# Kernel optimization log

Hardware: AMD Instinct MI355X
Metric: run time of the kernel (lower is better)

The kernel has to match this reference:

```python
import jax, jax.numpy as jnp
import numpy as np

D_MODEL = 1024
N_HEADS = 16


def setup_inputs() -> dict:
    key = jax.random.key(0)
    ks = jax.random.split(key, 11)
    B, S, D = 2, 2048, D_MODEL
    scale = 1.0 / np.sqrt(D)
    inp = {
        "q": jax.random.normal(ks[0], (B, S, D), jnp.float32),
        "k": jax.random.normal(ks[1], (B, S, D), jnp.float32),
        "v": jax.random.normal(ks[2], (B, S, D), jnp.float32),
        "W_q": jax.random.normal(ks[3], (D, D), jnp.float32) * scale,
        "b_q": jnp.zeros((D,), jnp.float32),
        "W_k": jax.random.normal(ks[4], (D, D), jnp.float32) * scale,
        "b_k": jnp.zeros((D,), jnp.float32),
        "W_v": jax.random.normal(ks[5], (D, D), jnp.float32) * scale,
        "b_v": jnp.zeros((D,), jnp.float32),
        "W_o": jax.random.normal(ks[6], (D, D), jnp.float32) * scale,
        "b_o": jnp.zeros((D,), jnp.float32),
    }
    return inp


def reference(q, k, v, W_q, b_q, W_k, b_k, W_v, b_v, W_o, b_o):
    B, S, D = q.shape
    H = N_HEADS
    d_k = D // H
    # linear projections, then split heads: [B, H, S, d_k]
    def proj(x, W, b):
        y = jnp.einsum("bsd,de->bse", x, W.T) + b
        return y.reshape(B, S, H, d_k).transpose(0, 2, 1, 3)
    Q = proj(q, W_q, b_q)
    K = proj(k, W_k, b_k)
    V = proj(v, W_v, b_v)
    # scaled dot-product attention with explicit [B,H,S,S] scores
    scores = jnp.einsum("bhqd,bhkd->bhqk", Q, K) / jnp.sqrt(jnp.float32(d_k))
    attn = jax.nn.softmax(scores, axis=-1)
    out = jnp.einsum("bhqk,bhkd->bhqd", attn, V)
    out = out.transpose(0, 2, 1, 3).reshape(B, S, D)
    return jnp.einsum("bsd,de->bse", out, W_o.T) + b_o
```

## Files before the change

kernel.cpp:

```cpp
#include <hip/hip_runtime.h>
#include <hip/hip_bf16.h>
#include <math.h>

typedef __bf16 bf16_t;
typedef bf16_t bf16x8 __attribute__((ext_vector_type(8)));
typedef float f32x4 __attribute__((ext_vector_type(4)));

#define D_MODEL 1024
#define NH 16
#define DK 64
#define SEQ 2048
#define MROWS 4096
#define LDSW 64
#define LDC 136

__device__ __forceinline__ bf16x8 ldfrag(const bf16_t* p) {
    union { uint4 u; bf16x8 v; } c;
    c.u = *reinterpret_cast<const uint4*>(p);
    return c.v;
}

__device__ __forceinline__ f32x4 zero4() { f32x4 z = {0.f, 0.f, 0.f, 0.f}; return z; }

__device__ __forceinline__ void gll16(const bf16_t* g, bf16_t* l) {
    __builtin_amdgcn_global_load_lds(
        (const __attribute__((address_space(1))) unsigned int*)g,
        (__attribute__((address_space(3))) unsigned int*)l,
        16, 0, 0);
}

__global__ void pack7(const float* __restrict__ q, const float* __restrict__ k,
                      const float* __restrict__ v, const float* __restrict__ wq,
                      const float* __restrict__ wk, const float* __restrict__ wv,
                      const float* __restrict__ wo,
                      bf16_t* __restrict__ dq, bf16_t* __restrict__ dk,
                      bf16_t* __restrict__ dv, bf16_t* __restrict__ dwq,
                      bf16_t* __restrict__ dwk, bf16_t* __restrict__ dwv,
                      bf16_t* __restrict__ dwo) {
    const int y = blockIdx.y;
    if (y >= 3 && blockIdx.x >= 1024) return;
    const float* s;
    bf16_t* d;
    switch (y) {
        case 0: s = q;  d = dq;  break;
        case 1: s = k;  d = dk;  break;
        case 2: s = v;  d = dv;  break;
        case 3: s = wq; d = dwq; break;
        case 4: s = wk; d = dwk; break;
        case 5: s = wv; d = dwv; break;
        default: s = wo; d = dwo; break;
    }
    int i = (blockIdx.x * blockDim.x + threadIdx.x) * 4;
    float4 f = *reinterpret_cast<const float4*>(s + i);
    union { bf16_t h[4]; uint2 u; } o;
    o.h[0] = (bf16_t)f.x; o.h[1] = (bf16_t)f.y; o.h[2] = (bf16_t)f.z; o.h[3] = (bf16_t)f.w;
    *reinterpret_cast<uint2*>(d + i) = o.u;
}

__device__ __forceinline__ void gemm_core(
    const bf16_t* __restrict__ A, const bf16_t* __restrict__ Bm,
    int K, int m0, int n0,
    bf16_t* As, bf16_t* Bs,
    f32x4 acc[4][4]) {

    const int tid = threadIdx.x;
    const int lane = tid & 63;
    const int wid = tid >> 6;
    const int wm = (wid >> 1) * 64, wn = (wid & 1) * 64;
    const int l15 = lane & 15, quad = lane >> 4;

    const int lrow   = lane >> 3;
    const int gcol   = ((lane & 7) ^ lrow) * 8;

    #pragma unroll
    for (int i = 0; i < 4; i++)
        #pragma unroll
        for (int j = 0; j < 4; j++) acc[i][j] = zero4();

    for (int k0 = 0; k0 < K; k0 += 64) {
        __syncthreads();
        #pragma unroll
        for (int t = 0; t < 4; t++) {
            const int rbase = wid * 32 + t * 8;
            gll16(A  + (size_t)(m0 + rbase + lrow) * K + k0 + gcol, As + rbase * LDSW);
            gll16(Bm + (size_t)(n0 + rbase + lrow) * K + k0 + gcol, Bs + rbase * LDSW);
        }
        __syncthreads();
        #pragma unroll
        for (int c = 0; c < 2; c++) {
            bf16x8 af[4], bfr[4];
            #pragma unroll
            for (int i = 0; i < 4; i++) {
                const int row = wm + i * 16 + l15;
                const int pc = ((c * 4 + quad) ^ (l15 & 7)) * 8;
                af[i] = ldfrag(As + row * LDSW + pc);
            }
            #pragma unroll
            for (int j = 0; j < 4; j++) {
                const int row = wn + j * 16 + l15;
                const int pc = ((c * 4 + quad) ^ (l15 & 7)) * 8;
                bfr[j] = ldfrag(Bs + row * LDSW + pc);
            }
            #pragma unroll
            for (int i = 0; i < 4; i++)
                #pragma unroll
                for (int j = 0; j < 4; j++)
                    acc[i][j] = __builtin_amdgcn_mfma_f32_16x16x32_bf16(af[i], bfr[j], acc[i][j], 0, 0, 0);
        }
    }
}

__global__ __launch_bounds__(256, 3) void proj_gemm(
    const bf16_t* __restrict__ qb, const bf16_t* __restrict__ kb,
    const bf16_t* __restrict__ vb,
    const bf16_t* __restrict__ Wq, const bf16_t* __restrict__ Wk,
    const bf16_t* __restrict__ Wv,
    const float* __restrict__ bq, const float* __restrict__ bk, const float* __restrict__ bv,
    bf16_t* __restrict__ Qh, bf16_t* __restrict__ Kh, bf16_t* __restrict__ Vt) {

    __shared__ __align__(16) bf16_t sm[128 * LDC];
    bf16_t* As = sm;
    bf16_t* Bs = sm + 128 * LDSW;
    bf16_t (*Cs)[LDC] = reinterpret_cast<bf16_t(*)[LDC]>(sm);
    f32x4 acc[4][4];

    const int mode = blockIdx.z;
    const bf16_t* X = (mode == 0) ? qb : (mode == 1) ? kb : vb;
    const bf16_t* W = (mode == 0) ? Wq : (mode == 1) ? Wk : Wv;
    const float* bias = (mode == 0) ? bq : (mode == 1) ? bk : bv;
    const int m0 = blockIdx.y * 128, n0 = blockIdx.x * 128;

    gemm_core(X, W, D_MODEL, m0, n0, As, Bs, acc);

    const int tid = threadIdx.x, lane = tid & 63, wid = tid >> 6;
    const int wm = (wid >> 1) * 64, wn = (wid & 1) * 64;
    const int l15 = lane & 15, quad = lane >> 4;

    __syncthreads();
    if (mode != 2) {
        const float sc = (mode == 0) ? 0.125f * 1.44269504f : 1.0f;
        #pragma unroll
        for (int i = 0; i < 4; i++)
            #pragma unroll
            for (int j = 0; j < 4; j++)
                #pragma unroll
                for (int r = 0; r < 4; r++) {
                    int gn = n0 + wn + j * 16 + l15;
                    Cs[wm + i * 16 + quad * 4 + r][wn + j * 16 + l15] =
                        (bf16_t)((acc[i][j][r] + bias[gn]) * sc);
                }
    } else {
        #pragma unroll
        for (int i = 0; i < 4; i++)
            #pragma unroll
            for (int j = 0; j < 4; j++)
                #pragma unroll
                for (int r = 0; r < 4; r++) {
                    int gn = n0 + wn + j * 16 + l15;
                    Cs[wn + j * 16 + l15][wm + i * 16 + quad * 4 + r] =
                        (bf16_t)(acc[i][j][r] + bias[gn]);
                }
    }
    __syncthreads();

    #pragma unroll
    for (int c = tid; c < 2048; c += 256) {
        int row = c >> 4, col8 = (c & 15) << 3;
        uint4 val = *reinterpret_cast<const uint4*>(&Cs[row][col8]);
        if (mode != 2) {
            int gm = m0 + row, gn = n0 + col8;
            int b = gm >> 11, seq = gm & 2047;
            int h = gn >> 6, dk = gn & 63;
            bf16_t* dst = (mode == 0) ? Qh : Kh;
            *reinterpret_cast<uint4*>(dst + ((size_t)(b * NH + h) * SEQ + seq) * DK + dk) = val;
        } else {
            int gn = n0 + row, gm = m0 + col8;
            int b = gm >> 11, seq = gm & 2047;
            int h = gn >> 6, dk = gn & 63;
            *reinterpret_cast<uint4*>(Vt + ((size_t)(b * NH + h) * DK + dk) * SEQ + seq) = val;
        }
    }
}

__global__ __launch_bounds__(256, 2) void out_gemm(
    const bf16_t* __restrict__ Oc, const bf16_t* __restrict__ Wo,
    const float* __restrict__ bo, float* __restrict__ Cout) {

    __shared__ __align__(16) bf16_t As[64 * LDSW];
    __shared__ __align__(16) bf16_t Bs[128 * LDSW];
    f32x4 acc[2][4];
    const int m0 = blockIdx.y * 64, n0 = blockIdx.x * 128;

    const int tid = threadIdx.x;
    const int lane = tid & 63;
    const int wid = tid >> 6;
    const int wm = (wid >> 1) * 32, wn = (wid & 1) * 64;
    const int l15 = lane & 15, quad = lane >> 4;
    const int lrow = lane >> 3;
    const int gcol = ((lane & 7) ^ lrow) * 8;

    #pragma unroll
    for (int i = 0; i < 2; i++)
        #pragma unroll
        for (int j = 0; j < 4; j++) acc[i][j] = zero4();

    for (int k0 = 0; k0 < D_MODEL; k0 += 64) {
        __syncthreads();
        #pragma unroll
        for (int t = 0; t < 2; t++) {
            const int rbase = wid * 16 + t * 8;
            gll16(Oc + (size_t)(m0 + rbase + lrow) * D_MODEL + k0 + gcol, As + rbase * LDSW);
        }
        #pragma unroll
        for (int t = 0; t < 4; t++) {
            const int rbase = wid * 32 + t * 8;
            gll16(Wo + (size_t)(n0 + rbase + lrow) * D_MODEL + k0 + gcol, Bs + rbase * LDSW);
        }
        __syncthreads();
        #pragma unroll
        for (int c = 0; c < 2; c++) {
            bf16x8 af[2], bfr[4];
            #pragma unroll
            for (int i = 0; i < 2; i++) {
                const int row = wm + i * 16 + l15;
                const int pc = ((c * 4 + quad) ^ (l15 & 7)) * 8;
                af[i] = ldfrag(As + row * LDSW + pc);
            }
            #pragma unroll
            for (int j = 0; j < 4; j++) {
                const int row = wn + j * 16 + l15;
                const int pc = ((c * 4 + quad) ^ (l15 & 7)) * 8;
                bfr[j] = ldfrag(Bs + row * LDSW + pc);
            }
            #pragma unroll
            for (int i = 0; i < 2; i++)
                #pragma unroll
                for (int j = 0; j < 4; j++)
                    acc[i][j] = __builtin_amdgcn_mfma_f32_16x16x32_bf16(af[i], bfr[j], acc[i][j], 0, 0, 0);
        }
    }

    #pragma unroll
    for (int i = 0; i < 2; i++)
        #pragma unroll
        for (int j = 0; j < 4; j++)
            #pragma unroll
            for (int r = 0; r < 4; r++) {
                int gm = m0 + wm + i * 16 + quad * 4 + r;
                int gn = n0 + wn + j * 16 + l15;
                Cout[(size_t)gm * D_MODEL + gn] = acc[i][j][r] + bo[gn];
            }
}

__global__ __launch_bounds__(256) void attn_kernel(
    const bf16_t* __restrict__ Qh, const bf16_t* __restrict__ Kh,
    const bf16_t* __restrict__ Vt, bf16_t* __restrict__ Oc) {

    __shared__ __align__(16) bf16_t Ks[64 * LDSW];
    __shared__ __align__(16) bf16_t Vts[64 * LDSW];
    __shared__ __align__(16) bf16_t Pls[64 * LDSW];

    const int tid = threadIdx.x, lane = tid & 63, wid = tid >> 6;
    const int l15 = lane & 15, quad = lane >> 4;
    const int bh = blockIdx.x;
    const int q0 = blockIdx.y * 64;
    const bf16_t* Qbase = Qh + (size_t)bh * SEQ * DK;
    const bf16_t* Kbase = Kh + (size_t)bh * SEQ * DK;
    const bf16_t* Vbase = Vt + (size_t)bh * DK * SEQ;

    const int lrow = lane >> 3;
    const int gcol = ((lane & 7) ^ lrow) * 8;

    bf16x8 aQ[2];
    #pragma unroll
    for (int c = 0; c < 2; c++)
        aQ[c] = ldfrag(Qbase + (size_t)(q0 + wid * 16 + l15) * DK + c * 32 + quad * 8);

    f32x4 oacc[4];
    #pragma unroll
    for (int j = 0; j < 4; j++) oacc[j] = zero4();
    float l_acc = 0.f;

    const int s7 = l15 & 7;
    bf16_t* prow = Pls + (wid * 16 + l15) * LDSW;

    for (int kt = 0; kt < SEQ / 64; kt++) {
        const int k0 = kt * 64;
        __syncthreads();
        #pragma unroll
        for (int t = 0; t < 2; t++) {
            const int rbase = wid * 16 + t * 8;
            gll16(Kbase + (size_t)(k0 + rbase + lrow) * DK + gcol,  Ks  + rbase * LDSW);
            gll16(Vbase + (size_t)(rbase + lrow) * SEQ + k0 + gcol, Vts + rbase * LDSW);
        }
        __syncthreads();

        f32x4 sacc[4];
        #pragma unroll
        for (int j = 0; j < 4; j++) sacc[j] = zero4();
        #pragma unroll
        for (int c = 0; c < 2; c++) {
            bf16x8 bk4[4];
            #pragma unroll
            for (int j = 0; j < 4; j++) {
                const int pc = ((c * 4 + quad) ^ s7) * 8;
                bk4[j] = ldfrag(Ks + (j * 16 + l15) * LDSW + pc);
            }
            #pragma unroll
            for (int j = 0; j < 4; j++)
                sacc[j] = __builtin_amdgcn_mfma_f32_16x16x32_bf16(
                    bk4[j], aQ[c], sacc[j], 0, 0, 0);
        }

        #pragma unroll
        for (int j = 0; j < 4; j++) {
            float e0 = exp2f(sacc[j][0]);
            float e1 = exp2f(sacc[j][1]);
            float e2 = exp2f(sacc[j][2]);
            float e3 = exp2f(sacc[j][3]);
            l_acc += (e0 + e1) + (e2 + e3);
            union { bf16_t h[4]; unsigned long long u; } pk;
            pk.h[0] = (bf16_t)e0; pk.h[1] = (bf16_t)e1;
            pk.h[2] = (bf16_t)e2; pk.h[3] = (bf16_t)e3;
            const int Lc = j * 2 + (quad >> 1);
            *reinterpret_cast<unsigned long long*>(
                prow + ((Lc ^ s7) << 3) + ((quad & 1) << 2)) = pk.u;
        }

        #pragma unroll
        for (int c = 0; c < 2; c++) {
            bf16x8 ap = ldfrag(prow + (((c * 4 + quad) ^ s7) << 3));
            bf16x8 bv4[4];
            #pragma unroll
            for (int j = 0; j < 4; j++) {
                const int pc = ((c * 4 + quad) ^ s7) * 8;
                bv4[j] = ldfrag(Vts + (j * 16 + l15) * LDSW + pc);
            }
            #pragma unroll
            for (int j = 0; j < 4; j++)
                oacc[j] = __builtin_amdgcn_mfma_f32_16x16x32_bf16(
                    ap, bv4[j], oacc[j], 0, 0, 0);
        }
    }

    float l = l_acc;
    l += __shfl_xor(l, 16, 64);
    l += __shfl_xor(l, 32, 64);

    const int pch = l15 >> 3, pwi = l15 & 7;
    #pragma unroll
    for (int r = 0; r < 4; r++) {
        float lr = __shfl(l, quad * 4 + r, 16);
        float inv = 1.0f / lr;
        bf16_t* orow = Pls + (wid * 16 + quad * 4 + r) * LDSW;
        const int rx = (quad * 4 + r) & 7;
        #pragma unroll
        for (int j = 0; j < 4; j++)
            orow[((pch + 2 * j) ^ rx) * 8 + pwi] = (bf16_t)(oacc[j][r] * inv);
    }
    __syncthreads();

    const int b = bh >> 4, h = bh & 15;
    #pragma unroll
    for (int c = tid; c < 512; c += 256) {
        int row = c >> 3, chunk = c & 7;
        uint4 val = *reinterpret_cast<const uint4*>(
            Pls + row * LDSW + ((chunk ^ (row & 7)) << 3));
        *reinterpret_cast<uint4*>(Oc + ((size_t)(b * SEQ + q0 + row)) * D_MODEL + h * DK + (chunk << 3)) = val;
    }
}

extern "C" void kernel_launch(void* const* d_in, const int* in_sizes, int n_in,
                              void* d_out, int out_size, void* d_ws, size_t ws_size,
                              hipStream_t stream) {
    const float* q  = (const float*)d_in[0];
    const float* k  = (const float*)d_in[1];
    const float* v  = (const float*)d_in[2];
    const float* Wq = (const float*)d_in[3];
    const float* bq = (const float*)d_in[4];
    const float* Wk = (const float*)d_in[5];
    const float* bk = (const float*)d_in[6];
    const float* Wv = (const float*)d_in[7];
    const float* bv = (const float*)d_in[8];
    const float* Wo = (const float*)d_in[9];
    const float* bo = (const float*)d_in[10];

    const size_t nx = (size_t)MROWS * D_MODEL;
    const size_t nw = (size_t)D_MODEL * D_MODEL;

    bf16_t* qb  = (bf16_t*)d_ws;
    bf16_t* kb  = qb  + nx;
    bf16_t* vb  = kb  + nx;
    bf16_t* Wqb = vb  + nx;
    bf16_t* Wkb = Wqb + nw;
    bf16_t* Wvb = Wkb + nw;
    bf16_t* Wob = Wvb + nw;
    bf16_t* Qh  = Wob + nw;
    bf16_t* Kh  = Qh  + nx;
    bf16_t* Vt  = Kh  + nx;
    bf16_t* Oc  = Vt  + nx;

    pack7<<<dim3(4096, 7), 256, 0, stream>>>(q, k, v, Wq, Wk, Wv, Wo,
                                             qb, kb, vb, Wqb, Wkb, Wvb, Wob);

    proj_gemm<<<dim3(8, 32, 3), 256, 0, stream>>>(qb, kb, vb, Wqb, Wkb, Wvb, bq, bk, bv, Qh, Kh, Vt);
    attn_kernel<<<dim3(32, 32), 256, 0, stream>>>(Qh, Kh, Vt, Oc);
    out_gemm<<<dim3(8, 64), 256, 0, stream>>>(Oc, Wob, bo, (float*)d_out);
}
```

Measured before the change: 239.6 us.

## Keep softmax probabilities in registers by permuting K rows to match MFMA layout

Loads K tile rows in a permuted order so the S^T accumulator layout matches the B-operand layout needed for the PV MFMA. The probability tile is then packed straight into registers instead of round-tripping through LDS. The PV product is computed transposed (V^T as A, P as B), which changes the output epilogue to per-lane row normalization. This removes per-iteration LDS writes and reads of P, at the cost of more intricate index math whose correctness depends on the permutation matching the MFMA register layout.

```diff
diff --git a/kernel.cpp b/kernel.cpp
--- a/kernel.cpp
+++ b/kernel.cpp
@@ -282,7 +282,6 @@
     float l_acc = 0.f;
 
     const int s7 = l15 & 7;
-    bf16_t* prow = Pls + (wid * 16 + l15) * LDSW;
 
     for (int kt = 0; kt < SEQ / 64; kt++) {
         const int k0 = kt * 64;
@@ -290,7 +289,10 @@
         #pragma unroll
         for (int t = 0; t < 2; t++) {
             const int rbase = wid * 16 + t * 8;
-            gll16(Kbase + (size_t)(k0 + rbase + lrow) * DK + gcol,  Ks  + rbase * LDSW);
+            const int srow = rbase + lrow;
+            const int sigma = ((srow >> 5) << 5) | (((srow >> 2) & 3) << 3) |
+                              (((srow >> 4) & 1) << 2) | (srow & 3);
+            gll16(Kbase + (size_t)(k0 + sigma) * DK + gcol,      Ks  + rbase * LDSW);
             gll16(Vbase + (size_t)(rbase + lrow) * SEQ + k0 + gcol, Vts + rbase * LDSW);
         }
         __syncthreads();
@@ -312,51 +314,57 @@
                     bk4[j], aQ[c], sacc[j], 0, 0, 0);
         }
 
-        #pragma unroll
-        for (int j = 0; j < 4; j++) {
-            float e0 = exp2f(sacc[j][0]);
-            float e1 = exp2f(sacc[j][1]);
-            float e2 = exp2f(sacc[j][2]);
-            float e3 = exp2f(sacc[j][3]);
-            l_acc += (e0 + e1) + (e2 + e3);
-            union { bf16_t h[4]; unsigned long long u; } pk;
-            pk.h[0] = (bf16_t)e0; pk.h[1] = (bf16_t)e1;
-            pk.h[2] = (bf16_t)e2; pk.h[3] = (bf16_t)e3;
-            const int Lc = j * 2 + (quad >> 1);
-            *reinterpret_cast<unsigned long long*>(
-                prow + ((Lc ^ s7) << 3) + ((quad & 1) << 2)) = pk.u;
-        }
-
+        bf16x8 pb[2];
         #pragma unroll
         for (int c = 0; c < 2; c++) {
-            bf16x8 ap = ldfrag(prow + (((c * 4 + quad) ^ s7) << 3));
-            bf16x8 bv4[4];
+            union { bf16_t h[8]; bf16x8 v; } pk;
+            #pragma unroll
+            for (int half = 0; half < 2; half++) {
+                const int j = c * 2 + half;
+                float e0 = exp2f(sacc[j][0]);
+                float e1 = exp2f(sacc[j][1]);
+                float e2 = exp2f(sacc[j][2]);
+                float e3 = exp2f(sacc[j][3]);
+                l_acc += (e0 + e1) + (e2 + e3);
+                pk.h[half * 4 + 0] = (bf16_t)e0;
+                pk.h[half * 4 + 1] = (bf16_t)e1;
+                pk.h[half * 4 + 2] = (bf16_t)e2;
+                pk.h[half * 4 + 3] = (bf16_t)e3;
+            }
+            pb[c] = pk.v;
+        }
+
+        #pragma unroll
+        for (int c = 0; c < 2; c++) {
+            bf16x8 av[4];
             #pragma unroll
             for (int j = 0; j < 4; j++) {
                 const int pc = ((c * 4 + quad) ^ s7) * 8;
-                bv4[j] = ldfrag(Vts + (j * 16 + l15) * LDSW + pc);
+                av[j] = ldfrag(Vts + (j * 16 + l15) * LDSW + pc);
             }
             #pragma unroll
             for (int j = 0; j < 4; j++)
                 oacc[j] = __builtin_amdgcn_mfma_f32_16x16x32_bf16(
-                    ap, bv4[j], oacc[j], 0, 0, 0);
+                    av[j], pb[c], oacc[j], 0, 0, 0);
         }
     }
 
     float l = l_acc;
     l += __shfl_xor(l, 16, 64);
     l += __shfl_xor(l, 32, 64);
-
-    const int pch = l15 >> 3, pwi = l15 & 7;
-    #pragma unroll
-    for (int r = 0; r < 4; r++) {
-        float lr = __shfl(l, quad * 4 + r, 16);
-        float inv = 1.0f / lr;
-        bf16_t* orow = Pls + (wid * 16 + quad * 4 + r) * LDSW;
-        const int rx = (quad * 4 + r) & 7;
-        #pragma unroll
-        for (int j = 0; j < 4; j++)
-            orow[((pch + 2 * j) ^ rx) * 8 + pwi] = (bf16_t)(oacc[j][r] * inv);
+    const float inv = 1.0f / l;
+
+    bf16_t* orow = Pls + (wid * 16 + l15) * LDSW;
+    #pragma unroll
+    for (int jp = 0; jp < 4; jp++) {
+        union { bf16_t h[4]; unsigned long long u; } pk;
+        pk.h[0] = (bf16_t)(oacc[jp][0] * inv);
+        pk.h[1] = (bf16_t)(oacc[jp][1] * inv);
+        pk.h[2] = (bf16_t)(oacc[jp][2] * inv);
+        pk.h[3] = (bf16_t)(oacc[jp][3] * inv);
+        const int Lc = jp * 2 + (quad >> 1);
+        *reinterpret_cast<unsigned long long*>(
+            orow + ((Lc ^ s7) << 3) + ((quad & 1) << 2)) = pk.u;
     }
     __syncthreads();
 
```

Result: no change. 235.1 us (-1.9%).
